# Optimization experiments

Measured on AMD Instinct MI355X. Metric: run time of the kernel, lower is better.

## Reference

```python
import jax, jax.numpy as jnp
import numpy as np

DIM = 1024
NUM_HEADS = 16
HEAD_DIM = DIM // NUM_HEADS
ROPE_THETA = 10000.0
EPS = float(jnp.finfo(jnp.float32).eps)  # torch RMSNorm default eps=None -> dtype eps


def rms_norm(x, w):
    # x: [..., d], w: [d]
    var = jnp.mean(x * x, axis=-1, keepdims=True)
    return x * jax.lax.rsqrt(var + EPS) * w


def rope(x, pos):
    # x: [b, h, n, d], pos: [b, n] int -> rotate-half RoPE
    d = x.shape[-1]
    inv_freq = 1.0 / (ROPE_THETA ** (jnp.arange(0, d, 2, dtype=jnp.float32) / d))  # [d/2]
    ang = pos.astype(jnp.float32)[:, None, :, None] * inv_freq  # [b, 1, n, d/2]
    cos = jnp.concatenate([jnp.cos(ang), jnp.cos(ang)], axis=-1)  # [b, 1, n, d]
    sin = jnp.concatenate([jnp.sin(ang), jnp.sin(ang)], axis=-1)
    x1, x2 = x[..., : d // 2], x[..., d // 2 :]
    rot = jnp.concatenate([-x2, x1], axis=-1)
    return x * cos + rot * sin


def setup_inputs() -> dict:
    key = jax.random.key(0)
    ks = jax.random.split(key, 9)
    b, n, m = 4, 2048, 2048
    s = 1.0 / np.sqrt(DIM)
    return {
        "tgt": jax.random.normal(ks[0], (b, n, DIM), jnp.float32),
        "src": jax.random.normal(ks[1], (b, m, DIM), jnp.float32),
        "tgt_pos": jax.random.randint(ks[2], (b, n), 0, 2048, jnp.int32),
        "src_pos": jax.random.randint(ks[3], (b, m), 0, 2048, jnp.int32),
        "Wq": jax.random.normal(ks[4], (DIM, DIM), jnp.float32) * s,
        "Wkv": jax.random.normal(ks[5], (DIM, 2 * DIM), jnp.float32) * s,
        "Wo": jax.random.normal(ks[6], (DIM, DIM), jnp.float32) * s,
        "q_norm_w": jnp.ones((HEAD_DIM,), jnp.float32),
        "k_norm_w": jnp.ones((HEAD_DIM,), jnp.float32),
    }


def reference(tgt, src, tgt_pos, src_pos, Wq, Wkv, Wo, q_norm_w, k_norm_w):
    b, n, _ = tgt.shape
    m = src.shape[1]
    h, d = NUM_HEADS, HEAD_DIM
    q = (tgt @ Wq).reshape(b, n, h, d).transpose(0, 2, 1, 3)  # [b,h,n,d]
    kv = (src @ Wkv).reshape(b, m, 2, h, d)
    k = kv[:, :, 0].transpose(0, 2, 1, 3)  # [b,h,m,d]
    v = kv[:, :, 1].transpose(0, 2, 1, 3)  # [b,h,m,d]
    q = rope(rms_norm(q, q_norm_w), tgt_pos)
    k = rope(rms_norm(k, k_norm_w), src_pos)
    scores = jnp.einsum("bhnd,bhmd->bhnm", q, k) / np.sqrt(d)
    attn = jax.nn.softmax(scores, axis=-1)
    x = jnp.einsum("bhnm,bhmd->bhnd", attn, v)  # [b,h,n,d]
    x = x.transpose(0, 2, 1, 3).reshape(b, n, h * d)
    return x @ Wo
```

## Files before the change

kernel.cpp:

```cpp
#include <hip/hip_runtime.h>


typedef __bf16 bf16_t;
typedef __bf16 bf16x8 __attribute__((ext_vector_type(8)));
typedef float  f32x4  __attribute__((ext_vector_type(4)));

#define DIMM   1024
#define NHEAD  16
#define HDIM   64
#define NB     4
#define SEQ    2048
#define NROWS  (NB * SEQ)
#define RMS_EPS 1.1920929e-07f
#define LOG2_10000_DIV32 0.4152410118609203f
#define QSCALE 0.18033688011112042f

__device__ __forceinline__ void async16(const bf16_t* g, bf16_t* l) {
    __builtin_amdgcn_global_load_lds(
        (const __attribute__((address_space(1))) void*)g,
        (__attribute__((address_space(3))) void*)l, 16, 0, 0);
}

__global__ __launch_bounds__(256)
void prep(const float* __restrict__ tgt, const float* __restrict__ src,
          bf16_t* __restrict__ tgtb, bf16_t* __restrict__ srcb,
          const float* __restrict__ Wq, const float* __restrict__ Wkv,
          const float* __restrict__ Wo, bf16_t* __restrict__ Wq_t,
          bf16_t* __restrict__ Wkv_t, bf16_t* __restrict__ Wo_t)
{
    __shared__ float t[32][33];
    int bid = blockIdx.x;
    if (bid < 8192) {
        const float* x;
        bf16_t* y;
        if (bid < 4096) { x = tgt; y = tgtb; }
        else            { bid -= 4096; x = src; y = srcb; }
        const size_t i = ((size_t)bid * 256 + threadIdx.x) * 8;
        float4 f0 = ((const float4*)(x + i))[0];
        float4 f1 = ((const float4*)(x + i))[1];
        bf16_t v[8];
        v[0] = (bf16_t)f0.x; v[1] = (bf16_t)f0.y; v[2] = (bf16_t)f0.z; v[3] = (bf16_t)f0.w;
        v[4] = (bf16_t)f1.x; v[5] = (bf16_t)f1.y; v[6] = (bf16_t)f1.z; v[7] = (bf16_t)f1.w;
        *(int4*)(y + i) = *(int4*)v;
        return;
    }
    bid -= 8192;
    const float* W; bf16_t* Wt; int N, nx;
    if (bid < 1024)      { W = Wq;  Wt = Wq_t;  N = 1024; nx = 32; }
    else if (bid < 3072) { bid -= 1024; W = Wkv; Wt = Wkv_t; N = 2048; nx = 64; }
    else                 { bid -= 3072; W = Wo;  Wt = Wo_t;  N = 1024; nx = 32; }
    const int K  = 1024;
    const int n0 = (bid % nx) * 32;
    const int k0 = (bid / nx) * 32;
    const int tx = threadIdx.x & 31;
    const int ty = threadIdx.x >> 5;
#pragma unroll
    for (int i = ty; i < 32; i += 8)
        t[i][tx] = W[(size_t)(k0 + i) * N + n0 + tx];
    __syncthreads();
#pragma unroll
    for (int i = ty; i < 32; i += 8)
        Wt[(size_t)(n0 + i) * K + k0 + tx] = (bf16_t)t[tx][i];
}

#define GEMM_MAIN_LOOP(A_, Bt_, K_, As, Bs)                                   \
    const int tid  = threadIdx.x;                                             \
    const int lane = tid & 63;                                                \
    const int wave = tid >> 6;                                                \
    const int wm   = (wave >> 1) * 64;                                        \
    const int wn   = (wave & 1) * 64;                                         \
    const int lr   = lane & 15;                                               \
    const int quad = lane >> 4;                                               \
    {                                                                         \
        const int srow = lane >> 3;                                           \
        const int sslot = lane & 7;                                           \
        unsigned aoff[4], boff[4];                                            \
        bf16_t *alp[4], *blp[4];                                              \
        _Pragma("unroll")                                                     \
        for (int t = 0; t < 4; ++t) {                                         \
            const int rb = wave * 32 + t * 8;                                 \
            const int r  = rb + srow;                                         \
            const int g  = sslot ^ (r & 7);                                   \
            aoff[t] = (unsigned)(bm + r) * (K_) + g * 8;                      \
            boff[t] = (unsigned)(bn + r) * (K_) + g * 8;                      \
            alp[t]  = (As) + rb * 64;                                         \
            blp[t]  = (Bs) + rb * 64;                                         \
        }                                                                     \
        for (int k0 = 0; k0 < (K_); k0 += 64) {                               \
            _Pragma("unroll")                                                 \
            for (int t = 0; t < 4; ++t) {                                     \
                async16((A_)  + (aoff[t] + k0), alp[t]);                      \
                async16((Bt_) + (boff[t] + k0), blp[t]);                      \
            }                                                                 \
            __syncthreads();                                                  \
            _Pragma("unroll")                                                 \
            for (int ks = 0; ks < 2; ++ks) {                                  \
                bf16x8 af[4], bfr[4];                                         \
                _Pragma("unroll")                                             \
                for (int i = 0; i < 4; ++i)                                   \
                    af[i] = *(const bf16x8*)&(As)[(wm + i * 16 + lr) * 64 +   \
                                (((ks * 4 + quad) ^ (lr & 7)) * 8)];          \
                _Pragma("unroll")                                             \
                for (int j = 0; j < 4; ++j)                                   \
                    bfr[j] = *(const bf16x8*)&(Bs)[(wn + j * 16 + lr) * 64 +  \
                                (((ks * 4 + quad) ^ (lr & 7)) * 8)];          \
                _Pragma("unroll")                                             \
                for (int i = 0; i < 4; ++i)                                   \
                    _Pragma("unroll")                                         \
                    for (int j = 0; j < 4; ++j)                               \
                        acc[i][j] = __builtin_amdgcn_mfma_f32_16x16x32_bf16(  \
                            af[i], bfr[j], acc[i][j], 0, 0, 0);               \
            }                                                                 \
            __syncthreads();                                                  \
        }                                                                     \
    }

__device__ __forceinline__ void norm_rope_store(
    f32x4 acc[4][4], const int* __restrict__ pos, const float* __restrict__ w,
    bf16_t* __restrict__ dstbase, int bm, int wm, int head,
    int lr, int quad, float oscale)
{
    float w0 = w[lr], w1 = w[16 + lr], w2 = w[32 + lr], w3 = w[48 + lr];
    const float invf0 = exp2f(-(float)lr * LOG2_10000_DIV32);
    const float invf1 = exp2f(-(float)(lr + 16) * LOG2_10000_DIV32);
#pragma unroll
    for (int i = 0; i < 4; ++i) {
        const int gr = bm + wm + i * 16 + quad * 4;
        int4 pos4 = *(const int4*)&pos[gr];
#pragma unroll
        for (int rg = 0; rg < 4; ++rg) {
            float x0 = acc[i][0][rg], x1 = acc[i][1][rg];
            float x2 = acc[i][2][rg], x3 = acc[i][3][rg];
            float ssum = x0 * x0 + x1 * x1 + x2 * x2 + x3 * x3;
#pragma unroll
            for (int off = 1; off < 16; off <<= 1)
                ssum += __shfl_xor(ssum, off, 64);
            const float rn = rsqrtf(ssum * (1.f / 64.f) + RMS_EPS);
            x0 *= rn * w0; x1 *= rn * w1; x2 *= rn * w2; x3 *= rn * w3;
            const float p  = (float)((&pos4.x)[rg]);
            const float a0 = p * invf0, a1 = p * invf1;
            const float s0 = __sinf(a0), c0 = __cosf(a0);
            const float s1 = __sinf(a1), c1 = __cosf(a1);
            const int row = gr + rg;
            const int bb = row >> 11, si = row & 2047;
            bf16_t* dst = dstbase +
                ((size_t)(bb * NHEAD + head) * SEQ + si) * HDIM;
            dst[lr]      = (bf16_t)((x0 * c0 - x2 * s0) * oscale);
            dst[16 + lr] = (bf16_t)((x1 * c1 - x3 * s1) * oscale);
            dst[32 + lr] = (bf16_t)((x2 * c0 + x0 * s0) * oscale);
            dst[48 + lr] = (bf16_t)((x3 * c1 + x1 * s1) * oscale);
        }
    }
}

__global__ __launch_bounds__(256, 4)
void gemm_qkv(const bf16_t* __restrict__ tgtb, const bf16_t* __restrict__ srcb,
              const bf16_t* __restrict__ Wq_t, const bf16_t* __restrict__ Wkv_t,
              const int* __restrict__ tpos, const int* __restrict__ spos,
              const float* __restrict__ qw, const float* __restrict__ kw,
              bf16_t* __restrict__ qb, bf16_t* __restrict__ kbuf,
              bf16_t* __restrict__ vT)
{
    __shared__ bf16_t As[128 * 64];
    __shared__ bf16_t Bs[128 * 64];
    const int raw = blockIdx.x;
    const int bid = (raw & 7) * 192 + (raw >> 3);
    if (bid < 512) {
        const int bm = (bid >> 3) * 128;
        const int bn = (bid & 7) * 128;
        f32x4 acc[4][4] = {};
        GEMM_MAIN_LOOP(tgtb, Wq_t, 1024, As, Bs)
        const int head = (bn + wn) >> 6;
        norm_rope_store(acc, tpos, qw, qb, bm, wm, head, lr, quad, QSCALE);
    } else {
        const int t2 = bid - 512;
        const int bm = (t2 >> 4) * 128;
        const int bn = (t2 & 15) * 128;
        f32x4 acc[4][4] = {};
        GEMM_MAIN_LOOP(srcb, Wkv_t, 1024, As, Bs)
        if (bn < 1024) {
            const int head = (bn + wn) >> 6;
            norm_rope_store(acc, spos, kw, kbuf, bm, wm, head, lr, quad, 1.0f);
        } else {
#pragma unroll
            for (int i = 0; i < 4; ++i) {
                const int M0 = bm + wm + i * 16;
                const int b  = M0 >> 11;
                const int mB = M0 & 2047;
                const int chunkbase = mB & ~127;
                const int ksm  = (mB >> 5) & 3;
                const int bit4 = (mB >> 4) & 1;
                const int pbase = (ksm * 4 + quad) * 8 + bit4 * 4;
#pragma unroll
                for (int j = 0; j < 4; ++j) {
                    const int c = bn + wn + j * 16 + lr - 1024;
                    const int h = c >> 6;
                    const int d = c & 63;
                    bf16_t pk[4];
#pragma unroll
                    for (int rg = 0; rg < 4; ++rg) pk[rg] = (bf16_t)acc[i][j][rg];
                    bf16_t* dst = vT + ((size_t)(b * NHEAD + h) * HDIM + d) * SEQ
                                  + chunkbase + pbase;
                    *(int2*)dst = *(int2*)pk;
                }
            }
        }
    }
}

__global__ __launch_bounds__(256, 4)
void gemm_o(const bf16_t* __restrict__ A, const bf16_t* __restrict__ Bt,
            float* __restrict__ Cp)
{
    __shared__ bf16_t As[128 * 64];
    __shared__ bf16_t Bs[128 * 64];
    const int raw = blockIdx.x;
    const int swz = (raw & 7) * 64 + (raw >> 3);
    const int bm = (swz >> 3) * 128;
    const int bn = (swz & 7) * 128;
    f32x4 acc[4][4] = {};
    GEMM_MAIN_LOOP(A, Bt, 1024, As, Bs)
#pragma unroll
    for (int i = 0; i < 4; ++i)
#pragma unroll
        for (int j = 0; j < 4; ++j) {
            const int r0 = bm + wm + i * 16 + quad * 4;
            const int c  = bn + wn + j * 16 + lr;
#pragma unroll
            for (int rg = 0; rg < 4; ++rg)
                Cp[(size_t)(r0 + rg) * 1024 + c] = acc[i][j][rg];
        }
}

__global__ __launch_bounds__(256, 4)
void attn(const bf16_t* __restrict__ q, const bf16_t* __restrict__ k,
          const bf16_t* __restrict__ vT, bf16_t* __restrict__ xo)
{
    __shared__ bf16_t Ks[2][64 * 64];
    __shared__ bf16_t Vs[2][64 * 64];

    const int bid = blockIdx.x;
    const int w   = bid >> 3;
    const int grp = (bid & 7) * 8 + (w >> 4);
    const int q0  = (w & 15) * 128;
    const int h   = grp & 15;
    const int b   = grp >> 4;
    const int bh  = b * NHEAD + h;

    const int tid  = threadIdx.x;
    const int lane = tid & 63;
    const int wv   = tid >> 6;
    const int lr   = lane & 15;
    const int quad = lane >> 4;

    const bf16_t* kb = k  + (size_t)bh * SEQ * HDIM;
    const bf16_t* vb = vT + (size_t)bh * HDIM * SEQ;

    bf16x8 aq[2][2];
#pragma unroll
    for (int t = 0; t < 2; ++t) {
        const bf16_t* qp = q + ((size_t)bh * SEQ + q0 + wv * 32 + t * 16 + lr) * HDIM;
        aq[t][0] = *(const bf16x8*)(qp + quad * 8);
        aq[t][1] = *(const bf16x8*)(qp + 32 + quad * 8);
    }

    bf16x8 vone;
#pragma unroll
    for (int i = 0; i < 8; ++i) vone[i] = (bf16_t)1.0f;

    size_t koff[2], voff[2];
    int lbase[2];
#pragma unroll
    for (int s = 0; s < 2; ++s) {
        const int rb = wv * 16 + s * 8;
        const int r  = rb + (lane >> 3);
        const int g  = (lane & 7) ^ (r & 7);
        koff[s]  = (size_t)r * HDIM + g * 8;
        voff[s]  = (size_t)r * SEQ  + g * 8;
        lbase[s] = rb * 64;
    }

    const bf16_t* kbase[2][2];
    const bf16_t* vbase[2][2];
#pragma unroll
    for (int bf = 0; bf < 2; ++bf)
#pragma unroll
        for (int x = 0; x < 2; ++x) {
            const int sw = (((x * 4 + quad) ^ (lr & 7)) * 8);
            kbase[bf][x] = &Ks[bf][lr * 64 + sw];
            vbase[bf][x] = &Vs[bf][lr * 64 + sw];
        }

    f32x4 zero4 = {0.f, 0.f, 0.f, 0.f};
    f32x4 o[2][4];
    f32x4 oex[2];
#pragma unroll
    for (int t = 0; t < 2; ++t) {
        oex[t] = zero4;
#pragma unroll
        for (int dt = 0; dt < 4; ++dt) o[t][dt] = zero4;
    }

#define STAGE(NB_, M0) do {                                                  \
    const size_t _kg = (size_t)(M0) * HDIM;                                  \
    async16(kb + _kg + koff[0], &Ks[NB_][lbase[0]]);                         \
    async16(kb + _kg + koff[1], &Ks[NB_][lbase[1]]);                         \
    async16(vb + (M0) + voff[0], &Vs[NB_][lbase[0]]);                        \
    async16(vb + (M0) + voff[1], &Vs[NB_][lbase[1]]);                        \
} while (0)

#define COMPUTE(CB) do {                                                     \
    _Pragma("unroll")                                                        \
    for (int ksm = 0; ksm < 2; ++ksm) {                                      \
        bf16x8 bp0, bp1;                                                     \
        _Pragma("unroll")                                                    \
        for (int half = 0; half < 2; ++half) {                               \
            const int mt = ksm * 2 + half;                                   \
            f32x4 s0 = zero4, s1 = zero4;                                    \
            bf16x8 ak0 = *(const bf16x8*)(kbase[CB][0] + mt * 1024);         \
            bf16x8 ak1 = *(const bf16x8*)(kbase[CB][1] + mt * 1024);         \
            __builtin_amdgcn_s_setprio(1);                                   \
            s0 = __builtin_amdgcn_mfma_f32_16x16x32_bf16(ak0, aq[0][0], s0, 0, 0, 0); \
            s1 = __builtin_amdgcn_mfma_f32_16x16x32_bf16(ak0, aq[1][0], s1, 0, 0, 0); \
            s0 = __builtin_amdgcn_mfma_f32_16x16x32_bf16(ak1, aq[0][1], s0, 0, 0, 0); \
            s1 = __builtin_amdgcn_mfma_f32_16x16x32_bf16(ak1, aq[1][1], s1, 0, 0, 0); \
            __builtin_amdgcn_s_setprio(0);                                   \
            _Pragma("unroll")                                                \
            for (int r = 0; r < 4; ++r) {                                    \
                bp0[half * 4 + r] = (bf16_t)__builtin_amdgcn_exp2f(s0[r]);   \
                bp1[half * 4 + r] = (bf16_t)__builtin_amdgcn_exp2f(s1[r]);   \
            }                                                                \
        }                                                                    \
        __builtin_amdgcn_s_setprio(1);                                       \
        _Pragma("unroll")                                                    \
        for (int dt = 0; dt < 4; ++dt) {                                     \
            bf16x8 av = *(const bf16x8*)(vbase[CB][ksm] + dt * 1024);        \
            o[0][dt] = __builtin_amdgcn_mfma_f32_16x16x32_bf16(av, bp0, o[0][dt], 0, 0, 0); \
            o[1][dt] = __builtin_amdgcn_mfma_f32_16x16x32_bf16(av, bp1, o[1][dt], 0, 0, 0); \
        }                                                                    \
        oex[0] = __builtin_amdgcn_mfma_f32_16x16x32_bf16(vone, bp0, oex[0], 0, 0, 0); \
        oex[1] = __builtin_amdgcn_mfma_f32_16x16x32_bf16(vone, bp1, oex[1], 0, 0, 0); \
        __builtin_amdgcn_s_setprio(0);                                       \
    }                                                                        \
} while (0)

    STAGE(0, 0);
    __syncthreads();

    for (int t0 = 0; t0 < 32; t0 += 2) {
        STAGE(1, (t0 + 1) * 64);
        COMPUTE(0);
        __syncthreads();
        STAGE(0, (((t0 + 2) & 31)) * 64);
        COMPUTE(1);
        __syncthreads();
    }

#undef STAGE
#undef COMPUTE

    float inv[2];
#pragma unroll
    for (int t = 0; t < 2; ++t) inv[t] = 1.f / oex[t][0];

#pragma unroll
    for (int t = 0; t < 2; ++t)
#pragma unroll
        for (int dt = 0; dt < 4; ++dt) {
            bf16_t pk[4];
#pragma unroll
            for (int rg = 0; rg < 4; ++rg)
                pk[rg] = (bf16_t)(o[t][dt][rg] * inv[t]);
            bf16_t* dst = xo + ((size_t)b * SEQ + q0 + wv * 32 + t * 16 + lr) * DIMM
                          + h * HDIM + dt * 16 + quad * 4;
            *(int2*)dst = *(int2*)pk;
        }
}

extern "C" void kernel_launch(void* const* d_in, const int* in_sizes, int n_in,
                              void* d_out, int out_size, void* d_ws, size_t ws_size,
                              hipStream_t stream)
{
    const float* tgt  = (const float*)d_in[0];
    const float* src  = (const float*)d_in[1];
    const int*   tpos = (const int*)d_in[2];
    const int*   spos = (const int*)d_in[3];
    const float* Wq   = (const float*)d_in[4];
    const float* Wkv  = (const float*)d_in[5];
    const float* Wo   = (const float*)d_in[6];
    const float* qw   = (const float*)d_in[7];
    const float* kw   = (const float*)d_in[8];
    float* out = (float*)d_out;

    char* ws = (char*)d_ws;
    const size_t MB = 1024 * 1024;
    bf16_t* Wq_t  = (bf16_t*)(ws + 0 * MB);
    bf16_t* Wkv_t = (bf16_t*)(ws + 2 * MB);
    bf16_t* Wo_t  = (bf16_t*)(ws + 6 * MB);
    bf16_t* tgtb  = (bf16_t*)(ws + 8 * MB);
    bf16_t* srcb  = (bf16_t*)(ws + 24 * MB);
    bf16_t* xb    = (bf16_t*)(ws + 24 * MB);
    bf16_t* qb    = (bf16_t*)(ws + 40 * MB);
    bf16_t* kbuf  = (bf16_t*)(ws + 56 * MB);
    bf16_t* vT    = (bf16_t*)(ws + 72 * MB);

    prep<<<12288, 256, 0, stream>>>(tgt, src, tgtb, srcb,
                                    Wq, Wkv, Wo, Wq_t, Wkv_t, Wo_t);

    gemm_qkv<<<1536, 256, 0, stream>>>(tgtb, srcb, Wq_t, Wkv_t,
                                       tpos, spos, qw, kw, qb, kbuf, vT);

    attn<<<1024, 256, 0, stream>>>(qb, kbuf, vT, xb);

    gemm_o<<<512, 256, 0, stream>>>(xb, Wo_t, out);
}
```

Before: 287.7 us.

## Double-buffer GEMM LDS tiles with K=32 stages to overlap loads and MFMA

Splits the GEMM main loop's 64-wide K tile into two 32-wide LDS buffers and ping-pongs between them. The async global-to-LDS load of the next stage is issued before computing on the current one, so load latency can hide behind MFMA work. LDS footprint stays the same. The price is one barrier per 32-K step instead of two per 64-K step, a narrower XOR swizzle (4 slots) that may raise bank conflicts, and a loop that assumes K is a multiple of 64.

```diff
diff --git a/kernel.cpp b/kernel.cpp
--- a/kernel.cpp
+++ b/kernel.cpp
@@ -72,45 +72,51 @@
     const int lr   = lane & 15;                                               \
     const int quad = lane >> 4;                                               \
     {                                                                         \
-        const int srow = lane >> 3;                                           \
-        const int sslot = lane & 7;                                           \
-        unsigned aoff[4], boff[4];                                            \
-        bf16_t *alp[4], *blp[4];                                              \
+        const int srow  = lane >> 2;                \
+        const int sslot = lane & 3;            \
+        unsigned aoff[2], boff[2];                                            \
+        int lbase[2];                                                         \
         _Pragma("unroll")                                                     \
-        for (int t = 0; t < 4; ++t) {                                         \
-            const int rb = wave * 32 + t * 8;                                 \
+        for (int t = 0; t < 2; ++t) {                                         \
+            const int rb = wave * 32 + t * 16;                                \
             const int r  = rb + srow;                                         \
-            const int g  = sslot ^ (r & 7);                                   \
-            aoff[t] = (unsigned)(bm + r) * (K_) + g * 8;                      \
-            boff[t] = (unsigned)(bn + r) * (K_) + g * 8;                      \
-            alp[t]  = (As) + rb * 64;                                         \
-            blp[t]  = (Bs) + rb * 64;                                         \
+            const int g  = sslot ^ (r & 3);                                   \
+            aoff[t]  = (unsigned)(bm + r) * (K_) + g * 8;                     \
+            boff[t]  = (unsigned)(bn + r) * (K_) + g * 8;                     \
+            lbase[t] = rb * 32;                                               \
         }                                                                     \
-        for (int k0 = 0; k0 < (K_); k0 += 64) {                               \
+        const int rdsw = (quad ^ (lr & 3)) * 8;                               \
+        auto STAGE_G = [&](int BUF, int KK) {                                 \
+            async16((A_)  + (aoff[0] + KK), &(As)[BUF][lbase[0]]);            \
+            async16((A_)  + (aoff[1] + KK), &(As)[BUF][lbase[1]]);            \
+            async16((Bt_) + (boff[0] + KK), &(Bs)[BUF][lbase[0]]);            \
+            async16((Bt_) + (boff[1] + KK), &(Bs)[BUF][lbase[1]]);            \
+        };                                                                    \
+        auto COMPUTE_G = [&](int BUF) {                                       \
+            bf16x8 af[4], bfr[4];                                             \
             _Pragma("unroll")                                                 \
-            for (int t = 0; t < 4; ++t) {                                     \
-                async16((A_)  + (aoff[t] + k0), alp[t]);                      \
-                async16((Bt_) + (boff[t] + k0), blp[t]);                      \
-            }                                                                 \
-            __syncthreads();                                                  \
+            for (int i = 0; i < 4; ++i)                                       \
+                af[i] = *(const bf16x8*)&(As)[BUF][(wm + i * 16 + lr) * 32 +  \
+                                                   rdsw];                     \
             _Pragma("unroll")                                                 \
-            for (int ks = 0; ks < 2; ++ks) {                                  \
-                bf16x8 af[4], bfr[4];                                         \
-                _Pragma("unroll")                                             \
-                for (int i = 0; i < 4; ++i)                                   \
-                    af[i] = *(const bf16x8*)&(As)[(wm + i * 16 + lr) * 64 +   \
-                                (((ks * 4 + quad) ^ (lr & 7)) * 8)];          \
+            for (int j = 0; j < 4; ++j)                                       \
+                bfr[j] = *(const bf16x8*)&(Bs)[BUF][(wn + j * 16 + lr) * 32 + \
+                                                    rdsw];                    \
+            _Pragma("unroll")                                                 \
+            for (int i = 0; i < 4; ++i)                                       \
                 _Pragma("unroll")                                             \
                 for (int j = 0; j < 4; ++j)                                   \
-                    bfr[j] = *(const bf16x8*)&(Bs)[(wn + j * 16 + lr) * 64 +  \
-                                (((ks * 4 + quad) ^ (lr & 7)) * 8)];          \
-                _Pragma("unroll")                                             \
-                for (int i = 0; i < 4; ++i)                                   \
-                    _Pragma("unroll")                                         \
-                    for (int j = 0; j < 4; ++j)                               \
-                        acc[i][j] = __builtin_amdgcn_mfma_f32_16x16x32_bf16(  \
-                            af[i], bfr[j], acc[i][j], 0, 0, 0);               \
-            }                                                                 \
+                    acc[i][j] = __builtin_amdgcn_mfma_f32_16x16x32_bf16(      \
+                        af[i], bfr[j], acc[i][j], 0, 0, 0);                   \
+        };                                                                    \
+        STAGE_G(0, 0);                                                        \
+        __syncthreads();                                                      \
+        for (int k = 32; k < (K_); k += 64) {                                 \
+            STAGE_G(1, k);                                                    \
+            COMPUTE_G(0);                                      \
+            __syncthreads();                                                  \
+            if (k + 32 < (K_)) STAGE_G(0, k + 32);                            \
+            COMPUTE_G(1);                                         \
             __syncthreads();                                                  \
         }                                                                     \
     }
@@ -161,8 +167,8 @@
               bf16_t* __restrict__ qb, bf16_t* __restrict__ kbuf,
               bf16_t* __restrict__ vT)
 {
-    __shared__ bf16_t As[128 * 64];
-    __shared__ bf16_t Bs[128 * 64];
+    __shared__ bf16_t As[2][128 * 32];
+    __shared__ bf16_t Bs[2][128 * 32];
     const int raw = blockIdx.x;
     const int bid = (raw & 7) * 192 + (raw >> 3);
     if (bid < 512) {
@@ -212,8 +218,8 @@
 void gemm_o(const bf16_t* __restrict__ A, const bf16_t* __restrict__ Bt,
             float* __restrict__ Cp)
 {
-    __shared__ bf16_t As[128 * 64];
-    __shared__ bf16_t Bs[128 * 64];
+    __shared__ bf16_t As[2][128 * 32];
+    __shared__ bf16_t Bs[2][128 * 32];
     const int raw = blockIdx.x;
     const int swz = (raw & 7) * 64 + (raw >> 3);
     const int bm = (swz >> 3) * 128;
```

After: 298.1 us. 3.6% more time.
